# Kernel tuning notes

Measured on AMD Instinct MI355X. Metric: run time of the kernel, lower is better.

The kernel has to match this reference:

```python
import jax, jax.numpy as jnp
import numpy as np
import math

NUM_HEADS = 4


def setup_inputs() -> dict:
    key = jax.random.key(0)
    k1, k2, k3, k4 = jax.random.split(key, 4)
    b, c, f, t = 8, 512, 32, 64
    x = jax.random.normal(k1, (b, c, f, t), dtype=jnp.float32)
    # Conv1d(k=1) weights stored as 2D (out, in); fan-in scaled like torch default
    qkv_w = jax.random.normal(k2, (3 * c, c), dtype=jnp.float32) / math.sqrt(c)
    qkv_b = jax.random.normal(k3, (3 * c,), dtype=jnp.float32) * 0.02
    proj_w = jax.random.normal(k4, (c, c), dtype=jnp.float32) / math.sqrt(c)
    proj_b = jnp.zeros((c,), dtype=jnp.float32)
    return {"x": x, "qkv_w": qkv_w, "qkv_b": qkv_b, "proj_w": proj_w, "proj_b": proj_b}


def reference(x, qkv_w, qkv_b, proj_w, proj_b):
    b, c, f, t = x.shape
    T = f * t
    xr = x.reshape(b, c, T)  # [b, c, T]
    # Note: original forward computes PositionalEncoding2D(x) but discards it.
    qkv = jnp.einsum('oc,bct->bot', qkv_w, xr) + qkv_b[None, :, None]  # [b, 3c, T]
    H = NUM_HEADS
    ch = c // H
    q, k, v = jnp.split(qkv, 3, axis=1)  # each [b, c, T]
    q = q.reshape(b * H, ch, T)
    k = k.reshape(b * H, ch, T)
    v = v.reshape(b * H, ch, T)
    scale = 1.0 / math.sqrt(math.sqrt(ch))
    w = jnp.einsum('bct,bcs->bts', q * scale, k * scale)  # [b*H, T, T]
    w = jax.nn.softmax(w.astype(jnp.float32), axis=-1).astype(q.dtype)
    a = jnp.einsum('bts,bcs->bct', w, v).reshape(b, c, T)
    h = jnp.einsum('oc,bct->bot', proj_w, a) + proj_b[None, :, None]
    return (xr + h).reshape(b, c, f, t)
```

## Files before the change

### kernel.cpp

```cpp
#include <hip/hip_runtime.h>

#define DEV static __device__ __forceinline__

typedef __attribute__((ext_vector_type(8))) short short8;
typedef __attribute__((ext_vector_type(4))) float f32x4;
typedef __attribute__((ext_vector_type(16))) float f32x16;
typedef __attribute__((ext_vector_type(2))) unsigned int uint2v;

DEV unsigned short f2bf(float f) {
    union { float f; unsigned int u; } v; v.f = f;
    unsigned int u = v.u;
    unsigned int r = (u + 0x7fffu + ((u >> 16) & 1u)) >> 16;
    return (unsigned short)r;
}

DEV unsigned int cvtpk(float lo, float hi) {
    unsigned int r;
    asm("v_cvt_pk_bf16_f32 %0, %1, %2" : "=v"(r) : "v"(lo), "v"(hi));
    return r;
}

DEV float pl32_max(float v) {
    union { float f; unsigned u; } c; c.f = v;
    uint2v r = __builtin_amdgcn_permlane32_swap(c.u, c.u, false, false);
    union { unsigned u; float f; } a, b; a.u = r[0]; b.u = r[1];
    return fmaxf(a.f, b.f);
}
DEV float pl32_sum(float v) {
    union { float f; unsigned u; } c; c.f = v;
    uint2v r = __builtin_amdgcn_permlane32_swap(c.u, c.u, false, false);
    union { unsigned u; float f; } a, b; a.u = r[0]; b.u = r[1];
    return a.f + b.f;
}

DEV unsigned short* swp(unsigned short* base, int row, int col, int rs) {
    int a = ((row * rs + col) << 1) ^ ((row & 7) << 4);
    return (unsigned short*)((char*)base + a);
}

__global__ void prep_kernel(const float* __restrict__ qkv_w,
                            const float* __restrict__ proj_w,
                            unsigned short* __restrict__ Wq,
                            unsigned short* __restrict__ Wp) {
    int i = blockIdx.x * blockDim.x + threadIdx.x;
    int stride = gridDim.x * blockDim.x;
    for (int j = i; j < 1536 * 512; j += stride) Wq[j] = f2bf(qkv_w[j]);
    for (int j = i; j < 512 * 512;  j += stride) Wp[j] = f2bf(proj_w[j]);
}

__global__ __launch_bounds__(256) void transpose_kernel(const float* __restrict__ x,
                                                        unsigned short* __restrict__ Xt) {
    __shared__ unsigned char lt[64 * 128];
    int b  = blockIdx.z;
    int c0 = blockIdx.y * 64;
    int t0 = blockIdx.x * 64;
    int tid = threadIdx.x;
    int tx = tid & 15, cy0 = tid >> 4;
    for (int p = 0; p < 4; ++p) {
        int cy = cy0 + p * 16;
        const float* src = &x[((size_t)(b * 512 + c0 + cy)) * 2048 + t0 + tx * 4];
        f32x4 v = *(const f32x4*)src;
        unsigned long long pk = (unsigned long long)f2bf(v[0])
                              | ((unsigned long long)f2bf(v[1]) << 16)
                              | ((unsigned long long)f2bf(v[2]) << 32)
                              | ((unsigned long long)f2bf(v[3]) << 48);
        int addr = (cy * 128 + tx * 8) ^ ((cy & 7) << 4);
        *(unsigned long long*)(lt + addr) = pk;
    }
    __syncthreads();
    int c16 = (tid & 3) * 16, tr = tid >> 2;
    unsigned short buf[16];
    for (int i = 0; i < 16; ++i) {
        int c = c16 + i;
        int addr = (c * 128 + tr * 2) ^ ((c & 7) << 4);
        buf[i] = *(unsigned short*)(lt + addr);
    }
    unsigned short* dst = &Xt[((size_t)(b * 2048 + t0 + tr)) * 512 + c0 + c16];
    *(short8*)dst       = *(short8*)&buf[0];
    *(short8*)(dst + 8) = *(short8*)&buf[8];
}

#define LP 72

template <int ORIENT>
__global__ __launch_bounds__(256, 2) void gemm_qkv_kernel(
    const unsigned short* __restrict__ Wq,
    const unsigned short* __restrict__ Xt,
    const float* __restrict__ qkv_b,
    unsigned short* __restrict__ Qw,
    unsigned short* __restrict__ Kw,
    unsigned short* __restrict__ Vw) {
    __shared__ unsigned short Ws[128][LP];
    __shared__ unsigned short Bs[128][LP];
    int b  = blockIdx.z;
    int ot = (ORIENT == 0) ? blockIdx.y : (8 + blockIdx.y);
    int o0 = ot * 128, t0 = blockIdx.x * 128;
    int tid = threadIdx.x, lane = tid & 63, w = tid >> 6;
    int lr = lane >> 4, lc = lane & 15;
    int wr = (w >> 1) * 64, wc = (w & 1) * 64;
    f32x4 acc[4][4];
    for (int m = 0; m < 4; m++)
        for (int n = 0; n < 4; n++) acc[m][n] = (f32x4){0.f, 0.f, 0.f, 0.f};
    int srow = tid >> 3, soff = (tid & 7) * 8;
    for (int k0 = 0; k0 < 512; k0 += 64) {
        __syncthreads();
        for (int rr = srow; rr < 128; rr += 32) {
            *(short8*)&Ws[rr][soff] = *(const short8*)&Wq[(size_t)(o0 + rr) * 512 + k0 + soff];
            *(short8*)&Bs[rr][soff] = *(const short8*)&Xt[((size_t)(b * 2048) + t0 + rr) * 512 + k0 + soff];
        }
        __syncthreads();
        for (int kk = 0; kk < 64; kk += 32) {
            int kb = kk + lr * 8;
            short8 af[4], bfv[4];
            if (ORIENT == 0) {
                for (int m = 0; m < 4; m++) af[m]  = *(const short8*)&Bs[wr + m * 16 + lc][kb];
                for (int n = 0; n < 4; n++) bfv[n] = *(const short8*)&Ws[wc + n * 16 + lc][kb];
            } else {
                for (int m = 0; m < 4; m++) af[m]  = *(const short8*)&Ws[wr + m * 16 + lc][kb];
                for (int n = 0; n < 4; n++) bfv[n] = *(const short8*)&Bs[wc + n * 16 + lc][kb];
            }
            for (int m = 0; m < 4; m++)
                for (int n = 0; n < 4; n++)
                    acc[m][n] = __builtin_amdgcn_mfma_f32_16x16x32_bf16(af[m], bfv[n], acc[m][n], 0, 0, 0);
        }
    }
    const float scale = 0.29730177875068026f;
    for (int m = 0; m < 4; m++)
        for (int n = 0; n < 4; n++)
            for (int r = 0; r < 4; r++) {
                int row = wr + m * 16 + lr * 4 + r;
                int col = wc + n * 16 + lc;
                float val = acc[m][n][r];
                if (ORIENT == 0) {
                    int t = t0 + row;
                    int o = o0 + col;
                    val = (val + qkv_b[o]) * scale;
                    if (o < 512) {
                        int h = o >> 7, cc = o & 127;
                        Qw[((size_t)((b * 4 + h) * 2048 + t)) * 128 + cc] = f2bf(val);
                    } else {
                        int oo = o - 512;
                        int h = oo >> 7, cc = oo & 127;
                        Kw[((size_t)((b * 4 + h) * 2048 + t)) * 128 + cc] = f2bf(val);
                    }
                } else {
                    int o = o0 + row;
                    int t = t0 + col;
                    val += qkv_b[o];
                    int oo = o - 1024;
                    int h = oo >> 7, cc = oo & 127;
                    Vw[((size_t)((b * 4 + h) * 128 + cc)) * 2048 + t] = f2bf(val);
                }
            }
}

__global__ __launch_bounds__(512, 2) void attn_kernel(
    const unsigned short* __restrict__ Qw,
    const unsigned short* __restrict__ Kw,
    const unsigned short* __restrict__ Vw,
    unsigned short* __restrict__ Aw) {
    __shared__ unsigned short lds[32768];
    int bid = blockIdx.x;
    int bh = bid & 31;
    int t0 = (bid >> 5) * 256;
    int tid = threadIdx.x, lane = tid & 63, w = tid >> 6;
    int l31 = lane & 31, hi = lane >> 5;
    int qrow = w * 32;

    const unsigned short* Kbase = &Kw[(size_t)bh * 2048 * 128];
    const unsigned short* Vbase = &Vw[(size_t)bh * 128 * 2048];

    short8 qf[8];
    #pragma unroll
    for (int st = 0; st < 8; st++)
        qf[st] = *(const short8*)&Qw[((size_t)bh * 2048 + t0 + qrow + l31) * 128 + st * 16 + hi * 8];

    f32x16 oacc[4];
    #pragma unroll
    for (int ct = 0; ct < 4; ct++)
        #pragma unroll
        for (int i = 0; i < 16; i++) oacc[ct][i] = 0.f;
    float mst = -1e30f, lst = 0.f;

    int kr = tid >> 4, ko = (tid & 15) * 8;
    int vr = tid >> 3, vo = (tid & 7) * 8;

    short8 kreg[2], vreg[2];
    #pragma unroll
    for (int p = 0; p < 2; p++)
        kreg[p] = *(const short8*)&Kbase[(size_t)(kr + p * 32) * 128 + ko];
    #pragma unroll
    for (int p = 0; p < 2; p++)
        vreg[p] = *(const short8*)&Vbase[(size_t)(vr + p * 64) * 2048 + vo];

    for (int it = 0; it < 32; ++it) {
        int cur = it & 1;
        unsigned short* Kb = lds + cur * 8192;
        unsigned short* Vb = lds + 16384 + cur * 8192;
        #pragma unroll
        for (int p = 0; p < 2; p++) *(short8*)swp(Kb, kr + p * 32, ko, 128) = kreg[p];
        #pragma unroll
        for (int p = 0; p < 2; p++) *(short8*)swp(Vb, vr + p * 64, vo, 64) = vreg[p];
        if (it + 1 < 32) {
            int s1 = (it + 1) * 64;
            #pragma unroll
            for (int p = 0; p < 2; p++)
                kreg[p] = *(const short8*)&Kbase[(size_t)(s1 + kr + p * 32) * 128 + ko];
            #pragma unroll
            for (int p = 0; p < 2; p++)
                vreg[p] = *(const short8*)&Vbase[(size_t)(vr + p * 64) * 2048 + s1 + vo];
        }
        __syncthreads();

        f32x16 s0, s1v;
        #pragma unroll
        for (int i = 0; i < 16; i++) { s0[i] = 0.f; s1v[i] = 0.f; }
        __builtin_amdgcn_s_setprio(1);
        #pragma unroll
        for (int st = 0; st < 8; st++) {
            short8 k0 = *(const short8*)swp(Kb, l31,      st * 16 + hi * 8, 128);
            short8 k1 = *(const short8*)swp(Kb, 32 + l31, st * 16 + hi * 8, 128);
            s0  = __builtin_amdgcn_mfma_f32_32x32x16_bf16(k0, qf[st], s0, 0, 0, 0);
            s1v = __builtin_amdgcn_mfma_f32_32x32x16_bf16(k1, qf[st], s1v, 0, 0, 0);
        }
        __builtin_amdgcn_s_setprio(0);

        float m16[16];
        #pragma unroll
        for (int i = 0; i < 16; i++) m16[i] = fmaxf(s0[i], s1v[i]);
        #pragma unroll
        for (int sdt = 8; sdt > 0; sdt >>= 1)
            #pragma unroll
            for (int i = 0; i < 8; i++)
                if (i < sdt) m16[i] = fmaxf(m16[i], m16[i + sdt]);
        float mx = pl32_max(m16[0]);
        if (!__all(mx <= mst + 8.0f)) {
            float mnew = fmaxf(mst, mx);
            float resc = __expf(mst - mnew);
            mst = mnew;
            lst *= resc;
            #pragma unroll
            for (int ct = 0; ct < 4; ct++)
                #pragma unroll
                for (int i = 0; i < 16; i++) oacc[ct][i] *= resc;
        }
        float pe[32];
        #pragma unroll
        for (int i = 0; i < 16; i++) pe[i]      = __expf(s0[i]  - mst);
        #pragma unroll
        for (int i = 0; i < 16; i++) pe[16 + i] = __expf(s1v[i] - mst);
        float a16[16];
        #pragma unroll
        for (int i = 0; i < 16; i++) a16[i] = pe[i] + pe[16 + i];
        #pragma unroll
        for (int sdt = 8; sdt > 0; sdt >>= 1)
            #pragma unroll
            for (int i = 0; i < 8; i++)
                if (i < sdt) a16[i] = a16[i] + a16[i + sdt];
        lst += pl32_sum(a16[0]);

        short8 pf[4];
        #pragma unroll
        for (int st = 0; st < 4; st++) {
            unsigned X0 = cvtpk(pe[st * 8 + 0], pe[st * 8 + 1]);
            unsigned X1 = cvtpk(pe[st * 8 + 2], pe[st * 8 + 3]);
            unsigned Y0 = cvtpk(pe[st * 8 + 4], pe[st * 8 + 5]);
            unsigned Y1 = cvtpk(pe[st * 8 + 6], pe[st * 8 + 7]);
            uint2v r0 = __builtin_amdgcn_permlane32_swap(X0, Y0, false, false);
            uint2v r1 = __builtin_amdgcn_permlane32_swap(X1, Y1, false, false);
            union { unsigned u[4]; short8 s; } uu;
            uu.u[0] = r0[0];
            uu.u[1] = r1[0];
            uu.u[2] = r0[1];
            uu.u[3] = r1[1];
            pf[st] = uu.s;
        }

        __builtin_amdgcn_s_setprio(1);
        #pragma unroll
        for (int ct = 0; ct < 4; ct++)
            #pragma unroll
            for (int st = 0; st < 4; st++) {
                short8 va = *(const short8*)swp(Vb, ct * 32 + l31, st * 16 + hi * 8, 64);
                oacc[ct] = __builtin_amdgcn_mfma_f32_32x32x16_bf16(va, pf[st], oacc[ct], 0, 0, 0);
            }
        __builtin_amdgcn_s_setprio(0);
    }

    __syncthreads();
    unsigned short* ep = lds + w * 4096;
    float invl = 1.f / lst;
    #pragma unroll
    for (int ct = 0; ct < 4; ct++)
        #pragma unroll
        for (int i = 0; i < 8; i++) {
            int c = (2 * i & 3) + 8 * (i >> 1) + 4 * hi + 32 * ct;
            unsigned d = cvtpk(oacc[ct][2 * i] * invl, oacc[ct][2 * i + 1] * invl);
            *(unsigned*)swp(ep, l31, c, 128) = d;
        }
    asm volatile("" ::: "memory");
    int q = lane >> 1, hf = lane & 1;
    int b = bh >> 2, h = bh & 3;
    #pragma unroll
    for (int p = 0; p < 8; p++) {
        short8 v = *(const short8*)swp(ep, q, hf * 64 + p * 8, 128);
        *(short8*)&Aw[((size_t)(b * 2048) + t0 + qrow + q) * 512 + h * 128 + hf * 64 + p * 8] = v;
    }
}

__global__ __launch_bounds__(256, 2) void gemm_proj_kernel(
    const unsigned short* __restrict__ Wp,
    const unsigned short* __restrict__ Aw,
    const float* __restrict__ proj_b,
    const float* __restrict__ x,
    float* __restrict__ out) {
    __shared__ unsigned short Ws[128][LP];
    __shared__ unsigned short Bs[128][LP];
    int b  = blockIdx.z;
    int o0 = blockIdx.y * 128, t0 = blockIdx.x * 128;
    int tid = threadIdx.x, lane = tid & 63, w = tid >> 6;
    int lr = lane >> 4, lc = lane & 15;
    int wr = (w >> 1) * 64, wc = (w & 1) * 64;
    f32x4 acc[4][4];
    for (int m = 0; m < 4; m++)
        for (int n = 0; n < 4; n++) acc[m][n] = (f32x4){0.f, 0.f, 0.f, 0.f};
    int srow = tid >> 3, soff = (tid & 7) * 8;
    for (int k0 = 0; k0 < 512; k0 += 64) {
        __syncthreads();
        for (int rr = srow; rr < 128; rr += 32) {
            *(short8*)&Ws[rr][soff] = *(const short8*)&Wp[(size_t)(o0 + rr) * 512 + k0 + soff];
            *(short8*)&Bs[rr][soff] = *(const short8*)&Aw[((size_t)(b * 2048) + t0 + rr) * 512 + k0 + soff];
        }
        __syncthreads();
        for (int kk = 0; kk < 64; kk += 32) {
            int kb = kk + lr * 8;
            short8 af[4], bfv[4];
            for (int m = 0; m < 4; m++) af[m]  = *(const short8*)&Ws[wr + m * 16 + lc][kb];
            for (int n = 0; n < 4; n++) bfv[n] = *(const short8*)&Bs[wc + n * 16 + lc][kb];
            for (int m = 0; m < 4; m++)
                for (int n = 0; n < 4; n++)
                    acc[m][n] = __builtin_amdgcn_mfma_f32_16x16x32_bf16(af[m], bfv[n], acc[m][n], 0, 0, 0);
        }
    }
    for (int m = 0; m < 4; m++)
        for (int n = 0; n < 4; n++)
            for (int r = 0; r < 4; r++) {
                int o = o0 + wr + m * 16 + lr * 4 + r;
                int t = t0 + wc + n * 16 + lc;
                size_t idx = ((size_t)(b * 512) + o) * 2048 + t;
                out[idx] = x[idx] + acc[m][n][r] + proj_b[o];
            }
}

extern "C" void kernel_launch(void* const* d_in, const int* in_sizes, int n_in,
                              void* d_out, int out_size, void* d_ws, size_t ws_size,
                              hipStream_t stream) {
    const float* x      = (const float*)d_in[0];
    const float* qkv_w  = (const float*)d_in[1];
    const float* qkv_b  = (const float*)d_in[2];
    const float* proj_w = (const float*)d_in[3];
    const float* proj_b = (const float*)d_in[4];
    float* out = (float*)d_out;

    unsigned short* ws = (unsigned short*)d_ws;
    unsigned short* Wq = ws;
    unsigned short* Wp = Wq + (size_t)1536 * 512;
    unsigned short* Xt = Wp + (size_t)512 * 512;
    unsigned short* Qw = Xt + (size_t)8 * 2048 * 512;
    unsigned short* Kw = Qw + (size_t)32 * 2048 * 128;
    unsigned short* Vw = Kw + (size_t)32 * 2048 * 128;
    unsigned short* Aw = Vw + (size_t)32 * 2048 * 128;

    prep_kernel<<<dim3(512), dim3(256), 0, stream>>>(qkv_w, proj_w, Wq, Wp);
    transpose_kernel<<<dim3(32, 8, 8), dim3(256), 0, stream>>>(x, Xt);
    gemm_qkv_kernel<0><<<dim3(16, 8, 8), dim3(256), 0, stream>>>(Wq, Xt, qkv_b, Qw, Kw, Vw);
    gemm_qkv_kernel<1><<<dim3(16, 4, 8), dim3(256), 0, stream>>>(Wq, Xt, qkv_b, Qw, Kw, Vw);
    attn_kernel<<<dim3(256), dim3(512), 0, stream>>>(Qw, Kw, Vw, Aw);
    gemm_proj_kernel<<<dim3(16, 4, 8), dim3(256), 0, stream>>>(Wp, Aw, proj_b, x, out);
}
```

Baseline: 171.0 us.

## Double-buffer GEMM tiles with register prefetch; split attention into smaller blocks

Both GEMM kernels now use double-buffered LDS tiles. The next K-slab is prefetched into registers while MFMAs run on the current slab, and the two full syncthreads are replaced by an lgkmcnt wait plus a raw barrier. The attention kernel moves from 512-thread blocks covering 256 query rows to 256-thread blocks covering 128 rows. This doubles the grid to 512 blocks for better CU occupancy and load balance, and each thread stages twice as many K/V vectors. The GEMM change doubles LDS use and raises register pressure. Each attention K/V tile is now loaded by twice as many blocks.

```diff
diff --git a/kernel.cpp b/kernel.cpp
--- a/kernel.cpp
+++ b/kernel.cpp
@@ -36,6 +36,11 @@
 DEV unsigned short* swp(unsigned short* base, int row, int col, int rs) {
     int a = ((row * rs + col) << 1) ^ ((row & 7) << 4);
     return (unsigned short*)((char*)base + a);
+}
+
+DEV void lds_barrier() {
+    asm volatile("s_waitcnt lgkmcnt(0)" ::: "memory");
+    __builtin_amdgcn_s_barrier();
 }
 
 __global__ void prep_kernel(const float* __restrict__ qkv_w,
@@ -90,8 +95,8 @@
     unsigned short* __restrict__ Qw,
     unsigned short* __restrict__ Kw,
     unsigned short* __restrict__ Vw) {
-    __shared__ unsigned short Ws[128][LP];
-    __shared__ unsigned short Bs[128][LP];
+    __shared__ unsigned short Ws[2][128][LP];
+    __shared__ unsigned short Bs[2][128][LP];
     int b  = blockIdx.z;
     int ot = (ORIENT == 0) ? blockIdx.y : (8 + blockIdx.y);
     int o0 = ot * 128, t0 = blockIdx.x * 128;
@@ -102,27 +107,44 @@
     for (int m = 0; m < 4; m++)
         for (int n = 0; n < 4; n++) acc[m][n] = (f32x4){0.f, 0.f, 0.f, 0.f};
     int srow = tid >> 3, soff = (tid & 7) * 8;
-    for (int k0 = 0; k0 < 512; k0 += 64) {
-        __syncthreads();
-        for (int rr = srow; rr < 128; rr += 32) {
-            *(short8*)&Ws[rr][soff] = *(const short8*)&Wq[(size_t)(o0 + rr) * 512 + k0 + soff];
-            *(short8*)&Bs[rr][soff] = *(const short8*)&Xt[((size_t)(b * 2048) + t0 + rr) * 512 + k0 + soff];
-        }
-        __syncthreads();
+
+    short8 wreg[4], breg[4];
+    #pragma unroll
+    for (int p = 0; p < 4; p++) {
+        wreg[p] = *(const short8*)&Wq[(size_t)(o0 + srow + p * 32) * 512 + soff];
+        breg[p] = *(const short8*)&Xt[((size_t)(b * 2048) + t0 + srow + p * 32) * 512 + soff];
+    }
+    for (int t = 0; t < 8; ++t) {
+        int cur = t & 1;
+        #pragma unroll
+        for (int p = 0; p < 4; p++) {
+            *(short8*)&Ws[cur][srow + p * 32][soff] = wreg[p];
+            *(short8*)&Bs[cur][srow + p * 32][soff] = breg[p];
+        }
+        if (t < 7) {
+            int k1 = (t + 1) * 64;
+            #pragma unroll
+            for (int p = 0; p < 4; p++) {
+                wreg[p] = *(const short8*)&Wq[(size_t)(o0 + srow + p * 32) * 512 + k1 + soff];
+                breg[p] = *(const short8*)&Xt[((size_t)(b * 2048) + t0 + srow + p * 32) * 512 + k1 + soff];
+            }
+        }
+        lds_barrier();
         for (int kk = 0; kk < 64; kk += 32) {
             int kb = kk + lr * 8;
             short8 af[4], bfv[4];
             if (ORIENT == 0) {
-                for (int m = 0; m < 4; m++) af[m]  = *(const short8*)&Bs[wr + m * 16 + lc][kb];
-                for (int n = 0; n < 4; n++) bfv[n] = *(const short8*)&Ws[wc + n * 16 + lc][kb];
+                for (int m = 0; m < 4; m++) af[m]  = *(const short8*)&Bs[cur][wr + m * 16 + lc][kb];
+                for (int n = 0; n < 4; n++) bfv[n] = *(const short8*)&Ws[cur][wc + n * 16 + lc][kb];
             } else {
-                for (int m = 0; m < 4; m++) af[m]  = *(const short8*)&Ws[wr + m * 16 + lc][kb];
-                for (int n = 0; n < 4; n++) bfv[n] = *(const short8*)&Bs[wc + n * 16 + lc][kb];
+                for (int m = 0; m < 4; m++) af[m]  = *(const short8*)&Ws[cur][wr + m * 16 + lc][kb];
+                for (int n = 0; n < 4; n++) bfv[n] = *(const short8*)&Bs[cur][wc + n * 16 + lc][kb];
             }
             for (int m = 0; m < 4; m++)
                 for (int n = 0; n < 4; n++)
                     acc[m][n] = __builtin_amdgcn_mfma_f32_16x16x32_bf16(af[m], bfv[n], acc[m][n], 0, 0, 0);
         }
+        __builtin_amdgcn_s_barrier();
     }
     const float scale = 0.29730177875068026f;
     for (int m = 0; m < 4; m++)
@@ -154,7 +176,7 @@
             }
 }
 
-__global__ __launch_bounds__(512, 2) void attn_kernel(
+__global__ __launch_bounds__(256, 2) void attn_kernel(
     const unsigned short* __restrict__ Qw,
     const unsigned short* __restrict__ Kw,
     const unsigned short* __restrict__ Vw,
@@ -162,7 +184,7 @@
     __shared__ unsigned short lds[32768];
     int bid = blockIdx.x;
     int bh = bid & 31;
-    int t0 = (bid >> 5) * 256;
+    int t0 = (bid >> 5) * 128;
     int tid = threadIdx.x, lane = tid & 63, w = tid >> 6;
     int l31 = lane & 31, hi = lane >> 5;
     int qrow = w * 32;
@@ -185,32 +207,32 @@
     int kr = tid >> 4, ko = (tid & 15) * 8;
     int vr = tid >> 3, vo = (tid & 7) * 8;
 
-    short8 kreg[2], vreg[2];
-    #pragma unroll
-    for (int p = 0; p < 2; p++)
-        kreg[p] = *(const short8*)&Kbase[(size_t)(kr + p * 32) * 128 + ko];
-    #pragma unroll
-    for (int p = 0; p < 2; p++)
-        vreg[p] = *(const short8*)&Vbase[(size_t)(vr + p * 64) * 2048 + vo];
+    short8 kreg[4], vreg[4];
+    #pragma unroll
+    for (int p = 0; p < 4; p++)
+        kreg[p] = *(const short8*)&Kbase[(size_t)(kr + p * 16) * 128 + ko];
+    #pragma unroll
+    for (int p = 0; p < 4; p++)
+        vreg[p] = *(const short8*)&Vbase[(size_t)(vr + p * 32) * 2048 + vo];
 
     for (int it = 0; it < 32; ++it) {
         int cur = it & 1;
         unsigned short* Kb = lds + cur * 8192;
         unsigned short* Vb = lds + 16384 + cur * 8192;
         #pragma unroll
-        for (int p = 0; p < 2; p++) *(short8*)swp(Kb, kr + p * 32, ko, 128) = kreg[p];
-        #pragma unroll
-        for (int p = 0; p < 2; p++) *(short8*)swp(Vb, vr + p * 64, vo, 64) = vreg[p];
+        for (int p = 0; p < 4; p++) *(short8*)swp(Kb, kr + p * 16, ko, 128) = kreg[p];
+        #pragma unroll
+        for (int p = 0; p < 4; p++) *(short8*)swp(Vb, vr + p * 32, vo, 64) = vreg[p];
         if (it + 1 < 32) {
             int s1 = (it + 1) * 64;
             #pragma unroll
-            for (int p = 0; p < 2; p++)
-                kreg[p] = *(const short8*)&Kbase[(size_t)(s1 + kr + p * 32) * 128 + ko];
-            #pragma unroll
-            for (int p = 0; p < 2; p++)
-                vreg[p] = *(const short8*)&Vbase[(size_t)(vr + p * 64) * 2048 + s1 + vo];
-        }
-        __syncthreads();
+            for (int p = 0; p < 4; p++)
+                kreg[p] = *(const short8*)&Kbase[(size_t)(s1 + kr + p * 16) * 128 + ko];
+            #pragma unroll
+            for (int p = 0; p < 4; p++)
+                vreg[p] = *(const short8*)&Vbase[(size_t)(vr + p * 32) * 2048 + s1 + vo];
+        }
+        lds_barrier();
 
         f32x16 s0, s1v;
         #pragma unroll
@@ -314,8 +336,8 @@
     const float* __restrict__ proj_b,
     const float* __restrict__ x,
     float* __restrict__ out) {
-    __shared__ unsigned short Ws[128][LP];
-    __shared__ unsigned short Bs[128][LP];
+    __shared__ unsigned short Ws[2][128][LP];
+    __shared__ unsigned short Bs[2][128][LP];
     int b  = blockIdx.z;
     int o0 = blockIdx.y * 128, t0 = blockIdx.x * 128;
     int tid = threadIdx.x, lane = tid & 63, w = tid >> 6;
@@ -325,22 +347,39 @@
     for (int m = 0; m < 4; m++)
         for (int n = 0; n < 4; n++) acc[m][n] = (f32x4){0.f, 0.f, 0.f, 0.f};
     int srow = tid >> 3, soff = (tid & 7) * 8;
-    for (int k0 = 0; k0 < 512; k0 += 64) {
-        __syncthreads();
-        for (int rr = srow; rr < 128; rr += 32) {
-            *(short8*)&Ws[rr][soff] = *(const short8*)&Wp[(size_t)(o0 + rr) * 512 + k0 + soff];
-            *(short8*)&Bs[rr][soff] = *(const short8*)&Aw[((size_t)(b * 2048) + t0 + rr) * 512 + k0 + soff];
-        }
-        __syncthreads();
+
+    short8 wreg[4], breg[4];
+    #pragma unroll
+    for (int p = 0; p < 4; p++) {
+        wreg[p] = *(const short8*)&Wp[(size_t)(o0 + srow + p * 32) * 512 + soff];
+        breg[p] = *(const short8*)&Aw[((size_t)(b * 2048) + t0 + srow + p * 32) * 512 + soff];
+    }
+    for (int t = 0; t < 8; ++t) {
+        int cur = t & 1;
+        #pragma unroll
+        for (int p = 0; p < 4; p++) {
+            *(short8*)&Ws[cur][srow + p * 32][soff] = wreg[p];
+            *(short8*)&Bs[cur][srow + p * 32][soff] = breg[p];
+        }
+        if (t < 7) {
+            int k1 = (t + 1) * 64;
+            #pragma unroll
+            for (int p = 0; p < 4; p++) {
+                wreg[p] = *(const short8*)&Wp[(size_t)(o0 + srow + p * 32) * 512 + k1 + soff];
+                breg[p] = *(const short8*)&Aw[((size_t)(b * 2048) + t0 + srow + p * 32) * 512 + k1 + soff];
+            }
+        }
+        lds_barrier();
         for (int kk = 0; kk < 64; kk += 32) {
             int kb = kk + lr * 8;
             short8 af[4], bfv[4];
-            for (int m = 0; m < 4; m++) af[m]  = *(const short8*)&Ws[wr + m * 16 + lc][kb];
-            for (int n = 0; n < 4; n++) bfv[n] = *(const short8*)&Bs[wc + n * 16 + lc][kb];
+            for (int m = 0; m < 4; m++) af[m]  = *(const short8*)&Ws[cur][wr + m * 16 + lc][kb];
+            for (int n = 0; n < 4; n++) bfv[n] = *(const short8*)&Bs[cur][wc + n * 16 + lc][kb];
             for (int m = 0; m < 4; m++)
                 for (int n = 0; n < 4; n++)
                     acc[m][n] = __builtin_amdgcn_mfma_f32_16x16x32_bf16(af[m], bfv[n], acc[m][n], 0, 0, 0);
         }
+        __builtin_amdgcn_s_barrier();
     }
     for (int m = 0; m < 4; m++)
         for (int n = 0; n < 4; n++)
@@ -375,6 +414,6 @@
     transpose_kernel<<<dim3(32, 8, 8), dim3(256), 0, stream>>>(x, Xt);
     gemm_qkv_kernel<0><<<dim3(16, 8, 8), dim3(256), 0, stream>>>(Wq, Xt, qkv_b, Qw, Kw, Vw);
     gemm_qkv_kernel<1><<<dim3(16, 4, 8), dim3(256), 0, stream>>>(Wq, Xt, qkv_b, Qw, Kw, Vw);
-    attn_kernel<<<dim3(256), dim3(512), 0, stream>>>(Qw, Kw, Vw, Aw);
+    attn_kernel<<<dim3(512), dim3(256), 0, stream>>>(Qw, Kw, Vw, Aw);
     gemm_proj_kernel<<<dim3(16, 4, 8), dim3(256), 0, stream>>>(Wp, Aw, proj_b, x, out);
 }
```

Measured after the change: 167.0 us. 1.02x faster.
